# Performance work log

Measured on AMD Instinct MI355X. Metric: run time of the kernel, lower is better.

Reference implementation:

```python
import jax, jax.numpy as jnp
import numpy as np

T, D, E, F = 8192, 1024, 8, 3584


def setup_inputs() -> dict:
    key = jax.random.key(0)
    ks = jax.random.split(key, 5)
    scale_in = 1.0 / np.sqrt(D)
    scale_ff = 1.0 / np.sqrt(F)
    return {
        "x": jax.random.normal(ks[0], (T, D), dtype=jnp.float32),
        "w1": jax.random.normal(ks[1], (E, F, D), dtype=jnp.float32) * scale_in,
        "w3": jax.random.normal(ks[2], (E, F, D), dtype=jnp.float32) * scale_in,
        "w2": jax.random.normal(ks[3], (E, D, F), dtype=jnp.float32) * scale_ff,
        "router_logits": jax.random.normal(ks[4], (T, E), dtype=jnp.float32),
        "top_k": 2,
    }


def reference(x, w1, w3, w2, router_logits, top_k):
    # Routing: softmax over experts, keep top-k, renormalize (Mixtral, normalize=True)
    probs = jax.nn.softmax(router_logits, axis=-1)            # [T, E]
    top_vals, top_idx = jax.lax.top_k(probs, top_k)           # [T, k]
    top_vals = top_vals / jnp.sum(top_vals, axis=-1, keepdims=True)
    tokens = jnp.arange(x.shape[0])[:, None]
    weights = jnp.zeros_like(probs).at[tokens, top_idx].set(top_vals)  # [T, E]

    gate = jnp.einsum('td,efd->tef', x, w1)                   # [T, E, F]
    up = jnp.einsum('td,efd->tef', x, w3)                     # [T, E, F]
    h = jax.nn.silu(gate) * up                                # [T, E, F]
    out = jnp.einsum('te,tef,edf->td', weights, h, w2)        # [T, D]
    return out
```

## Files before the change

### kernel.cpp

```cpp
#include <hip/hip_runtime.h>
#include <cstdint>

#define T_TOK 8192
#define D_DIM 1024
#define E_EXP 8
#define F_DIM 3584
#define NROW  (2 * T_TOK)
#define PROWS_PAD 18432
#define MAXTILES 72
#define MAXBANDS 18

typedef __attribute__((ext_vector_type(8))) __bf16 bf16x8;
typedef __attribute__((ext_vector_type(4))) float f32x4;

__device__ __forceinline__ void gload16(const void* g, void* l) {
    __builtin_amdgcn_global_load_lds(
        (const __attribute__((address_space(1))) void*)(g),
        (__attribute__((address_space(3))) void*)(l),
        16, 0, 0);
}

__global__ void cvt_kernel(const float* __restrict__ in, __bf16* __restrict__ out, long n) {
    long i = ((long)blockIdx.x * blockDim.x + threadIdx.x) * 8;
    if (i >= n) return;
    const float4 f0 = *(const float4*)(in + i);
    const float4 f1 = *(const float4*)(in + i + 4);
    bf16x8 o;
    o[0] = (__bf16)f0.x; o[1] = (__bf16)f0.y; o[2] = (__bf16)f0.z; o[3] = (__bf16)f0.w;
    o[4] = (__bf16)f1.x; o[5] = (__bf16)f1.y; o[6] = (__bf16)f1.z; o[7] = (__bf16)f1.w;
    *(bf16x8*)(out + i) = o;
}

__global__ void route_kernel(const float* __restrict__ rl, int* cnt,
                             int* __restrict__ eidx, float* __restrict__ ewgt) {
    int t = blockIdx.x * blockDim.x + threadIdx.x;
    if (t >= T_TOK) return;
    float l[8];
#pragma unroll
    for (int e = 0; e < 8; ++e) l[e] = rl[t * 8 + e];
    int i0 = 0; float v0 = l[0];
    int i1 = -1; float v1 = -1e30f;
#pragma unroll
    for (int e = 1; e < 8; ++e) {
        if (l[e] > v0) { v1 = v0; i1 = i0; v0 = l[e]; i0 = e; }
        else if (l[e] > v1) { v1 = l[e]; i1 = e; }
    }
    float wsec = 1.f / (1.f + __expf(v0 - v1));
    eidx[2 * t] = i0; eidx[2 * t + 1] = i1;
    ewgt[2 * t] = 1.f - wsec; ewgt[2 * t + 1] = wsec;
    atomicAdd(&cnt[i0], 1); atomicAdd(&cnt[i1], 1);
}

__global__ void scan_kernel(const int* __restrict__ cnt, int* __restrict__ pofs) {
    if (threadIdx.x == 0) {
        int a = 0;
        for (int e = 0; e < E_EXP; ++e) { pofs[e] = a; a += (cnt[e] + 255) & ~255; }
        pofs[E_EXP] = a;
    }
}

__global__ void tiles_kernel(const int* __restrict__ pofs, int* __restrict__ tile_e,
                             int* __restrict__ tile_r0, int* __restrict__ meta) {
    if (threadIdx.x == 0) {
        int n = 0;
        for (int e = 0; e < E_EXP; ++e)
            for (int r = pofs[e]; r < pofs[e + 1]; r += 256) {
                tile_e[n] = e; tile_r0[n] = r; ++n;
            }
        meta[0] = n;
    }
}

__global__ void assign_kernel(const int* __restrict__ eidx, const int* __restrict__ pofs,
                              int* cnt2, int* __restrict__ tokOf, int* __restrict__ rowOf) {
    int t = blockIdx.x * blockDim.x + threadIdx.x;
    if (t >= T_TOK) return;
#pragma unroll
    for (int s = 0; s < 2; ++s) {
        int e = eidx[2 * t + s];
        int pos = atomicAdd(&cnt2[e], 1);
        int prow = pofs[e] + pos;
        tokOf[prow] = t;
        rowOf[2 * t + s] = prow;
    }
}

__global__ void gather_kernel(const float* __restrict__ x, const int* __restrict__ tokOf,
                              __bf16* __restrict__ xg) {
    const int idx = blockIdx.x * blockDim.x + threadIdx.x;
    const int pr = idx >> 7;
    const int j = (idx & 127) * 8;
    const int tk = tokOf[pr];
    bf16x8 o = {};
    if (tk >= 0) {
        const float4 f0 = *(const float4*)(x + (long)tk * D_DIM + j);
        const float4 f1 = *(const float4*)(x + (long)tk * D_DIM + j + 4);
        o[0] = (__bf16)f0.x; o[1] = (__bf16)f0.y; o[2] = (__bf16)f0.z; o[3] = (__bf16)f0.w;
        o[4] = (__bf16)f1.x; o[5] = (__bf16)f1.y; o[6] = (__bf16)f1.z; o[7] = (__bf16)f1.w;
    }
    *(bf16x8*)(xg + (long)pr * D_DIM + j) = o;
}

__device__ __forceinline__ int chunk_row(int c) { return ((c >> 7) << 4) | ((c >> 2) & 15); }
__device__ __forceinline__ int chunk_col(int c) {
    return ((c >> 6) & 1) * 32 + (((c & 3) * 8) ^ (((c >> 5) & 1) << 4));
}

template <int NT>
__device__ __forceinline__ void moe_pipeline(
    const __bf16* const (&srcA)[2][2], const __bf16* const (&srcB)[2][2],
    __bf16 (&Ash)[2][2][8192], __bf16 (&Bsh)[2][2][8192],
    int wave, int abase, int wm, int bh, int bsel, f32x4 (&acc)[8][4])
{
    auto stA = [&](int buf, int kt, int h) {
        const long k0 = (long)kt * 64;
        gload16(srcA[h][0] + k0, &Ash[buf][h][(0 * 512 + wave * 64) * 8]);
        gload16(srcA[h][1] + k0, &Ash[buf][h][(1 * 512 + wave * 64) * 8]);
    };
    auto stB = [&](int buf, int kt, int h) {
        const long k0 = (long)kt * 64;
        gload16(srcB[h][0] + k0, &Bsh[buf][h][(0 * 512 + wave * 64) * 8]);
        gload16(srcB[h][1] + k0, &Bsh[buf][h][(1 * 512 + wave * 64) * 8]);
    };

    bf16x8 bfr[4][2];
    bf16x8 afr[4][2];

#define LD_A4(Ab, h) \
    _Pragma("unroll") for (int j = 0; j < 4; ++j) { \
        afr[j][0] = *(const bf16x8*)((Ab) + ((4*(h)+j) * 2 + 0) * 512); \
        afr[j][1] = *(const bf16x8*)((Ab) + ((4*(h)+j) * 2 + 1) * 512); \
    }

#define LD_B(Bb) \
    _Pragma("unroll") for (int ni = 0; ni < 4; ++ni) { \
        bfr[ni][0] = *(const bf16x8*)((Bb) + ((bsel * 4 + ni) * 2 + 0) * 512); \
        bfr[ni][1] = *(const bf16x8*)((Bb) + ((bsel * 4 + ni) * 2 + 1) * 512); \
    }

#define MFMA_H(h) \
    _Pragma("unroll") for (int j = 0; j < 4; ++j) \
        _Pragma("unroll") for (int ni = 0; ni < 4; ++ni) { \
            acc[4*(h)+j][ni] = __builtin_amdgcn_mfma_f32_16x16x32_bf16(afr[j][0], bfr[ni][0], acc[4*(h)+j][ni], 0, 0, 0); \
            acc[4*(h)+j][ni] = __builtin_amdgcn_mfma_f32_16x16x32_bf16(afr[j][1], bfr[ni][1], acc[4*(h)+j][ni], 0, 0, 0); \
        }

#define PH_OPEN() \
    __builtin_amdgcn_sched_barrier(0); \
    __builtin_amdgcn_s_barrier(); \
    asm volatile("s_waitcnt lgkmcnt(0)" ::: "memory"); \
    __builtin_amdgcn_sched_barrier(0); \
    __builtin_amdgcn_s_setprio(1);

#define PH_CLOSE() \
    __builtin_amdgcn_s_setprio(0); \
    __builtin_amdgcn_sched_barrier(0); \
    __builtin_amdgcn_s_barrier(); \
    __builtin_amdgcn_sched_barrier(0);

#define PH_CLOSE_G(lastf) \
    __builtin_amdgcn_s_setprio(0); \
    __builtin_amdgcn_sched_barrier(0); \
    if (lastf) { asm volatile("s_waitcnt vmcnt(0)" ::: "memory"); } \
    else       { asm volatile("s_waitcnt vmcnt(4)" ::: "memory"); } \
    __builtin_amdgcn_s_barrier(); \
    __builtin_amdgcn_sched_barrier(0);

    stA(0, 0, 0); stA(0, 0, 1); stB(0, 0, 0); stB(0, 0, 1);
    stB(1, 1, 0); stB(1, 1, 1);
    asm volatile("s_waitcnt vmcnt(4)" ::: "memory");
    __builtin_amdgcn_s_barrier();

    const __bf16* AbE = &Ash[0][wm][abase];
    const __bf16* BbE = &Bsh[0][bh][abase];
    const __bf16* AbO = &Ash[1][wm][abase];
    const __bf16* BbO = &Bsh[1][bh][abase];

    for (int it = 0; it < NT / 2; ++it) {
        const int kv = 2 * it + 1;
        const bool last = (it == NT / 2 - 1);
        LD_A4(AbE, 0) LD_B(BbE)
        stA(1, kv, 0); stA(1, kv, 1);
        PH_OPEN() MFMA_H(0) PH_CLOSE()
        LD_A4(AbE, 1)
        if (!last) { stB(0, kv + 1, 0); stB(0, kv + 1, 1); }
        PH_OPEN() MFMA_H(1) PH_CLOSE_G(last)
        LD_A4(AbO, 0) LD_B(BbO)
        if (!last) { stA(0, kv + 1, 0); stA(0, kv + 1, 1); }
        PH_OPEN() MFMA_H(0) PH_CLOSE()
        LD_A4(AbO, 1)
        if (!last) { stB(1, kv + 2, 0); stB(1, kv + 2, 1); }
        PH_OPEN() MFMA_H(1) PH_CLOSE_G(last)
    }
#undef LD_A4
#undef LD_B
#undef MFMA_H
#undef PH_OPEN
#undef PH_CLOSE
#undef PH_CLOSE_G
}

__global__ __launch_bounds__(512, 1)
void gemm1_kernel(const __bf16* __restrict__ xg,
                  const __bf16* __restrict__ w1b,
                  const __bf16* __restrict__ w3b,
                  const int* __restrict__ tile_e,
                  const int* __restrict__ tile_r0,
                  const int* __restrict__ meta,
                  __bf16* __restrict__ h) {
    const int count = meta[0];
    const int bands = (count + 3) >> 2;
    const int live = bands * 112;
    const int bid = blockIdx.x;
    if (bid >= live) return;
    const int w = (bid & 7) * (live >> 3) + (bid >> 3);
    const int q28 = w / 28, r = w % 28;
    const int tile = (q28 >> 2) * 4 + r / 7;
    const int nt = (q28 & 3) * 7 + r % 7;
    if (tile >= count) return;
    const int e = tile_e[tile];
    const int row0 = tile_r0[tile];

    __shared__ __align__(16) __bf16 Ash[2][2][8192];
    __shared__ __align__(16) __bf16 Bsh[2][2][8192];

    const int tid = threadIdx.x;
    const int wave = tid >> 6, lane = tid & 63;
    const int wm = wave >> 2, wn = wave & 3;
    const int fr = lane & 15, fg = lane >> 4;

    const __bf16* srcA[2][2];
    const __bf16* srcB[2][2];
#pragma unroll
    for (int half = 0; half < 2; ++half)
#pragma unroll
        for (int j = 0; j < 2; ++j) {
            const int c = tid + j * 512;
            srcA[half][j] = xg + (long)(row0 + half * 128 + chunk_row(c)) * D_DIM + chunk_col(c);
            const int rb = half * 128 + chunk_row(c);
            const int blk = rb >> 4;
            const int f = nt * 128 + (blk >> 1) * 16 + (rb & 15);
            srcB[half][j] = ((blk & 1) ? w3b : w1b) + ((long)e * F_DIM + f) * D_DIM + chunk_col(c);
        }

    const int abase = fr * 32 + ((fg * 8) ^ ((fr & 8) << 1));
    f32x4 acc[8][4] = {};

    moe_pipeline<16>(srcA, srcB, Ash, Bsh, wave, abase, wm, wn >> 1, wn & 1, acc);

#pragma unroll
    for (int mi = 0; mi < 8; ++mi) {
#pragma unroll
        for (int reg = 0; reg < 4; ++reg) {
            const int lm = wm * 128 + mi * 16 + fg * 4 + reg;
            const long hrow = (long)(row0 + lm) * F_DIM;
#pragma unroll
            for (int b = 0; b < 2; ++b) {
                const float g = acc[mi][2 * b][reg];
                const float u = acc[mi][2 * b + 1][reg];
                const float s = g / (1.f + __expf(-g));
                h[hrow + nt * 128 + (wn * 2 + b) * 16 + fr] = (__bf16)(s * u);
            }
        }
    }
}

__global__ __launch_bounds__(512, 1)
void gemm2_kernel(const __bf16* __restrict__ hb,
                  const __bf16* __restrict__ w2b,
                  const int* __restrict__ tile_e,
                  const int* __restrict__ tile_r0,
                  const int* __restrict__ meta,
                  __bf16* __restrict__ o2p) {
    const int count = meta[0];
    const int bands = (count + 3) >> 2;
    const int live = bands * 32;
    const int bid = blockIdx.x;
    if (bid >= live) return;
    const int w = (bid & 7) * (live >> 3) + (bid >> 3);
    const int band = w >> 5, s = w & 31;
    const int tile = band * 4 + (s >> 3);
    const int nt = s & 3, ks = (s >> 2) & 1;
    if (tile >= count) return;
    const int e = tile_e[tile];
    const int row0 = tile_r0[tile];

    __shared__ __align__(16) __bf16 Ash[2][2][8192];
    __shared__ __align__(16) __bf16 Bsh[2][2][8192];

    const int tid = threadIdx.x;
    const int wave = tid >> 6, lane = tid & 63;
    const int wm = wave >> 2, wn = wave & 3;
    const int fr = lane & 15, fg = lane >> 4;
    const int kofs = ks * (F_DIM / 2);

    const __bf16* srcA[2][2];
    const __bf16* srcB[2][2];
#pragma unroll
    for (int half = 0; half < 2; ++half)
#pragma unroll
        for (int j = 0; j < 2; ++j) {
            const int c = tid + j * 512;
            srcA[half][j] = hb + (long)(row0 + half * 128 + chunk_row(c)) * F_DIM + kofs + chunk_col(c);
            const int rb = half * 128 + chunk_row(c);
            srcB[half][j] = w2b + ((long)e * D_DIM + nt * 256 + rb) * F_DIM + kofs + chunk_col(c);
        }

    const int abase = fr * 32 + ((fg * 8) ^ ((fr & 8) << 1));
    f32x4 acc[8][4] = {};

    moe_pipeline<28>(srcA, srcB, Ash, Bsh, wave, abase, wm, wn >> 1, wn & 1, acc);

    __bf16* ps = o2p + (long)ks * PROWS_PAD * D_DIM;
#pragma unroll
    for (int mi = 0; mi < 8; ++mi) {
#pragma unroll
        for (int reg = 0; reg < 4; ++reg) {
            const int lm = wm * 128 + mi * 16 + fg * 4 + reg;
            const long obase = (long)(row0 + lm) * D_DIM + nt * 256 + wn * 64 + fr;
#pragma unroll
            for (int ni = 0; ni < 4; ++ni)
                ps[obase + ni * 16] = (__bf16)acc[mi][ni][reg];
        }
    }
}

__global__ void combine_kernel(const __bf16* __restrict__ o2p, const int* __restrict__ rowOf,
                               const float* __restrict__ ewgt, float* __restrict__ out) {
    const int idx = blockIdx.x * blockDim.x + threadIdx.x;
    const int t = idx >> 7;
    const int j = (idx & 127) * 8;
    const long r0 = rowOf[2 * t], r1 = rowOf[2 * t + 1];
    const float w0 = ewgt[2 * t], w1 = ewgt[2 * t + 1];
    float r[8] = {0, 0, 0, 0, 0, 0, 0, 0};
#pragma unroll
    for (int s = 0; s < 2; ++s) {
        const bf16x8 a = *(const bf16x8*)(o2p + ((long)s * PROWS_PAD + r0) * D_DIM + j);
        const bf16x8 b = *(const bf16x8*)(o2p + ((long)s * PROWS_PAD + r1) * D_DIM + j);
#pragma unroll
        for (int q = 0; q < 8; ++q) r[q] += w0 * (float)a[q] + w1 * (float)b[q];
    }
    float4* ob = (float4*)(out + (long)t * D_DIM + j);
    ob[0] = make_float4(r[0], r[1], r[2], r[3]);
    ob[1] = make_float4(r[4], r[5], r[6], r[7]);
}

extern "C" void kernel_launch(void* const* d_in, const int* in_sizes, int n_in,
                              void* d_out, int out_size, void* d_ws, size_t ws_size,
                              hipStream_t stream) {
    const float* x  = (const float*)d_in[0];
    const float* w1 = (const float*)d_in[1];
    const float* w3 = (const float*)d_in[2];
    const float* w2 = (const float*)d_in[3];
    const float* rl = (const float*)d_in[4];
    float* out = (float*)d_out;

    char* ws = (char*)d_ws;
    size_t off = 0;
    auto alloc = [&](size_t bytes) {
        void* p = ws + off;
        off += (bytes + 255) & ~(size_t)255;
        return p;
    };
    __bf16* xg   = (__bf16*)alloc((size_t)PROWS_PAD * D_DIM * 2);
    __bf16* w1b  = (__bf16*)alloc((size_t)E_EXP * F_DIM * D_DIM * 2);
    __bf16* w3b  = (__bf16*)alloc((size_t)E_EXP * F_DIM * D_DIM * 2);
    __bf16* hbuf = (__bf16*)alloc((size_t)PROWS_PAD * F_DIM * 2);
    int*   tokOf = (int*)alloc(PROWS_PAD * 4);
    int*   rowOf = (int*)alloc(NROW * 4);
    int*   eidx  = (int*)alloc(NROW * 4);
    float* ewgt  = (float*)alloc(NROW * 4);
    int*   cnt1  = (int*)alloc(64);
    int*   cnt2  = (int*)alloc(64);
    int*   pofs  = (int*)alloc(64);
    int*   tileE = (int*)alloc(MAXTILES * 4 + 64);
    int*   tileR = (int*)alloc(MAXTILES * 4 + 64);
    int*   meta  = (int*)alloc(64);
    __bf16* w2b = (__bf16*)ws;
    __bf16* o2p = (__bf16*)(ws + (size_t)E_EXP * D_DIM * F_DIM * 2);

    hipMemsetAsync(cnt1, 0, 64, stream);
    hipMemsetAsync(cnt2, 0, 64, stream);
    hipMemsetAsync(tokOf, 0xFF, PROWS_PAD * 4, stream);

    route_kernel<<<T_TOK / 256, 256, 0, stream>>>(rl, cnt1, eidx, ewgt);
    scan_kernel<<<1, 64, 0, stream>>>(cnt1, pofs);
    tiles_kernel<<<1, 64, 0, stream>>>(pofs, tileE, tileR, meta);
    assign_kernel<<<T_TOK / 256, 256, 0, stream>>>(eidx, pofs, cnt2, tokOf, rowOf);
    gather_kernel<<<PROWS_PAD * 128 / 256, 256, 0, stream>>>(x, tokOf, xg);

    {
        const long n = (long)E_EXP * F_DIM * D_DIM;
        const int blks = (int)(n / 8 / 256);
        cvt_kernel<<<blks, 256, 0, stream>>>(w1, w1b, n);
        cvt_kernel<<<blks, 256, 0, stream>>>(w3, w3b, n);
    }

    gemm1_kernel<<<MAXBANDS * 112, 512, 0, stream>>>(xg, w1b, w3b, tileE, tileR, meta, hbuf);

    {
        const long n = (long)E_EXP * D_DIM * F_DIM;
        cvt_kernel<<<(int)(n / 8 / 256), 256, 0, stream>>>(w2, w2b, n);
    }

    gemm2_kernel<<<MAXBANDS * 32, 512, 0, stream>>>(hbuf, w2b, tileE, tileR, meta, o2p);

    combine_kernel<<<T_TOK * (D_DIM / 8) / 256, 256, 0, stream>>>(o2p, rowOf, ewgt, out);
}
```

Before: 689.0 us.

## Split MoE GEMM pipeline into finer quarter phases with deeper prefetch

Restructures the main loop of the shared MoE GEMM pipeline. Each k-step now runs four MFMA sub-phases of two A-rows each instead of two of four, and A fragments go into separate register sets so LDS reads for later sub-phases can overlap earlier MFMAs. Global-to-LDS loads are spread one half-tile per phase, and the prologue adds an extra A load so the vmcnt wait depth goes from 4 to 6. The intent is better overlap of LDS reads and global loads with MFMA work, at the cost of more barriers per k-step, more registers, and fragile hand-tuned waitcnt accounting.

```diff
diff --git a/kernel.cpp b/kernel.cpp
--- a/kernel.cpp
+++ b/kernel.cpp
@@ -124,12 +124,12 @@
     };
 
     bf16x8 bfr[4][2];
-    bf16x8 afr[4][2];
-
-#define LD_A4(Ab, h) \
-    _Pragma("unroll") for (int j = 0; j < 4; ++j) { \
-        afr[j][0] = *(const bf16x8*)((Ab) + ((4*(h)+j) * 2 + 0) * 512); \
-        afr[j][1] = *(const bf16x8*)((Ab) + ((4*(h)+j) * 2 + 1) * 512); \
+    bf16x8 a01[2][2], a23[2][2], a45[2][2], a67[2][2];
+
+#define LD_A2(dst, Ab, p) \
+    _Pragma("unroll") for (int j = 0; j < 2; ++j) { \
+        dst[j][0] = *(const bf16x8*)((Ab) + ((2*(p)+j) * 2 + 0) * 512); \
+        dst[j][1] = *(const bf16x8*)((Ab) + ((2*(p)+j) * 2 + 1) * 512); \
     }
 
 #define LD_B(Bb) \
@@ -138,11 +138,11 @@
         bfr[ni][1] = *(const bf16x8*)((Bb) + ((bsel * 4 + ni) * 2 + 1) * 512); \
     }
 
-#define MFMA_H(h) \
-    _Pragma("unroll") for (int j = 0; j < 4; ++j) \
+#define MFMA_P(p, src) \
+    _Pragma("unroll") for (int j = 0; j < 2; ++j) \
         _Pragma("unroll") for (int ni = 0; ni < 4; ++ni) { \
-            acc[4*(h)+j][ni] = __builtin_amdgcn_mfma_f32_16x16x32_bf16(afr[j][0], bfr[ni][0], acc[4*(h)+j][ni], 0, 0, 0); \
-            acc[4*(h)+j][ni] = __builtin_amdgcn_mfma_f32_16x16x32_bf16(afr[j][1], bfr[ni][1], acc[4*(h)+j][ni], 0, 0, 0); \
+            acc[2*(p)+j][ni] = __builtin_amdgcn_mfma_f32_16x16x32_bf16(src[j][0], bfr[ni][0], acc[2*(p)+j][ni], 0, 0, 0); \
+            acc[2*(p)+j][ni] = __builtin_amdgcn_mfma_f32_16x16x32_bf16(src[j][1], bfr[ni][1], acc[2*(p)+j][ni], 0, 0, 0); \
         }
 
 #define PH_OPEN() \
@@ -162,13 +162,13 @@
     __builtin_amdgcn_s_setprio(0); \
     __builtin_amdgcn_sched_barrier(0); \
     if (lastf) { asm volatile("s_waitcnt vmcnt(0)" ::: "memory"); } \
-    else       { asm volatile("s_waitcnt vmcnt(4)" ::: "memory"); } \
+    else       { asm volatile("s_waitcnt vmcnt(6)" ::: "memory"); } \
     __builtin_amdgcn_s_barrier(); \
     __builtin_amdgcn_sched_barrier(0);
 
-    stA(0, 0, 0); stA(0, 0, 1); stB(0, 0, 0); stB(0, 0, 1);
-    stB(1, 1, 0); stB(1, 1, 1);
-    asm volatile("s_waitcnt vmcnt(4)" ::: "memory");
+    stB(0, 0, 0); stB(0, 0, 1); stA(0, 0, 0); stA(0, 0, 1);
+    stB(1, 1, 0); stB(1, 1, 1); stA(1, 1, 0);
+    asm volatile("s_waitcnt vmcnt(6)" ::: "memory");
     __builtin_amdgcn_s_barrier();
 
     const __bf16* AbE = &Ash[0][wm][abase];
@@ -177,24 +177,36 @@
     const __bf16* BbO = &Bsh[1][bh][abase];
 
     for (int it = 0; it < NT / 2; ++it) {
-        const int kv = 2 * it + 1;
+        const int v = 2 * it + 1, ku = 2 * it + 2, kv = 2 * it + 3;
         const bool last = (it == NT / 2 - 1);
-        LD_A4(AbE, 0) LD_B(BbE)
-        stA(1, kv, 0); stA(1, kv, 1);
-        PH_OPEN() MFMA_H(0) PH_CLOSE()
-        LD_A4(AbE, 1)
-        if (!last) { stB(0, kv + 1, 0); stB(0, kv + 1, 1); }
-        PH_OPEN() MFMA_H(1) PH_CLOSE_G(last)
-        LD_A4(AbO, 0) LD_B(BbO)
-        if (!last) { stA(0, kv + 1, 0); stA(0, kv + 1, 1); }
-        PH_OPEN() MFMA_H(0) PH_CLOSE()
-        LD_A4(AbO, 1)
-        if (!last) { stB(1, kv + 2, 0); stB(1, kv + 2, 1); }
-        PH_OPEN() MFMA_H(1) PH_CLOSE_G(last)
-    }
-#undef LD_A4
+        LD_A2(a01, AbE, 0) LD_B(BbE)
+        stA(1, v, 1);
+        asm volatile("s_waitcnt lgkmcnt(8)" ::: "memory");
+        PH_OPEN() MFMA_P(0, a01) PH_CLOSE()
+        LD_A2(a23, AbE, 1)
+        if (!last) stB(0, ku, 0);
+        PH_OPEN() MFMA_P(1, a23) PH_CLOSE()
+        LD_A2(a45, AbE, 2) LD_A2(a67, AbE, 3)
+        if (!last) stB(0, ku, 1);
+        PH_OPEN() MFMA_P(2, a45) PH_CLOSE()
+        if (!last) stA(0, ku, 0);
+        PH_OPEN() MFMA_P(3, a67) PH_CLOSE_G(last)
+        LD_A2(a01, AbO, 0) LD_B(BbO)
+        if (!last) stA(0, ku, 1);
+        asm volatile("s_waitcnt lgkmcnt(8)" ::: "memory");
+        PH_OPEN() MFMA_P(0, a01) PH_CLOSE()
+        LD_A2(a23, AbO, 1)
+        if (!last) stB(1, kv, 0);
+        PH_OPEN() MFMA_P(1, a23) PH_CLOSE()
+        LD_A2(a45, AbO, 2) LD_A2(a67, AbO, 3)
+        if (!last) stB(1, kv, 1);
+        PH_OPEN() MFMA_P(2, a45) PH_CLOSE()
+        if (!last) stA(1, kv, 0);
+        PH_OPEN() MFMA_P(3, a67) PH_CLOSE_G(last)
+    }
+#undef LD_A2
 #undef LD_B
-#undef MFMA_H
+#undef MFMA_P
 #undef PH_OPEN
 #undef PH_CLOSE
 #undef PH_CLOSE_G
```

New measurement: 696.7 us. Within noise of the previous version (+1.1%).
